# Kernel tuning notes

Hardware: AMD Instinct MI355X
Metric: run time of the kernel (lower is better)

Reference implementation:

```python
import jax, jax.numpy as jnp
import numpy as np

B, N, C, CO = 256, 80, 1024, 1024
SLOPE = 0.2
BN_EPS = 1e-5

def leaky(x):
    return jax.nn.leaky_relu(x, SLOPE)

def setup_inputs() -> dict:
    key = jax.random.key(0)
    ks = jax.random.split(key, 8)
    stdv = 1.0 / np.sqrt(C)
    return {
        "x": jax.random.normal(ks[0], (B, N, C), jnp.float32),
        "out1": jax.random.normal(ks[1], (B, N), jnp.float32),
        "A": jax.random.uniform(ks[2], (N, N), jnp.float32, 0.05, 1.0),
        "static_weight": jax.random.uniform(ks[3], (C, C), jnp.float32, -stdv, stdv),
        "conv_g_w": jax.random.normal(ks[4], (C, C), jnp.float32) * 0.02,
        "conv_g_b": jnp.zeros((C,), jnp.float32),
        "bn_gamma": jnp.ones((C,), jnp.float32),
        "bn_beta": jnp.zeros((C,), jnp.float32),
        "conv_co_w": jax.random.normal(ks[5], (N, 2 * C), jnp.float32) * 0.02,
        "conv_co_b": jnp.zeros((N,), jnp.float32),
        "dynamic_weight": jax.random.uniform(ks[6], (C, CO), jnp.float32, -stdv, stdv),
    }

def _gen_adj(A):
    # D = diag(rowsum(A)^-0.5); adj = (A @ D).T @ D = D A^T D
    d = jnp.power(A.sum(1), -0.5)
    return d[:, None] * A.T * d[None, :]

def _gen_adjs(A):
    # batched version of _gen_adj; A: [B,N,N]
    d = jnp.power(A.sum(2), -0.5)  # [B,N]
    return d[:, :, None] * jnp.swapaxes(A, 1, 2) * d[:, None, :]

def reference(x, out1, A, static_weight, conv_g_w, conv_g_b, bn_gamma, bn_beta, conv_co_w, conv_co_b, dynamic_weight):
    n = x.shape[1]
    # static GCN + residual
    adj_s = _gen_adj(A)
    h = leaky(jnp.einsum('ij,bjc->bic', adj_s, x))
    x = x + h @ static_weight
    # construct dynamic graph
    xt = jnp.swapaxes(x, 1, 2)                      # [B,C,N]
    glb = xt.mean(2)                                # adaptive avg pool -> [B,C]
    glb = glb @ conv_g_w.T + conv_g_b               # 1x1 conv
    mu = glb.mean(0)
    var = glb.var(0)                                # biased, training-mode BN
    glb = (glb - mu) * jax.lax.rsqrt(var + BN_EPS) * bn_gamma + bn_beta
    glb = leaky(glb)
    cat = jnp.concatenate([jnp.broadcast_to(glb[:, :, None], xt.shape), xt], axis=1)  # [B,2C,N]
    dyn = jax.nn.sigmoid(jnp.einsum('nk,bkm->bnm', conv_co_w, cat) + conv_co_b[None, :, None])  # [B,N,N]
    # adjacency consistency loss
    out1s = jax.nn.sigmoid(out1)
    t = jnp.einsum('bn,bnm->bm', out1s, dyn) / n
    loss = jnp.sum(jnp.linalg.norm(out1s - t, axis=1))
    # dynamic GCN
    adjs = _gen_adjs(dyn)
    h = leaky(jnp.einsum('bnm,bmc->bnc', adjs, x))
    out = leaky(h @ dynamic_weight)
    return out, loss
```

## Files before the change

### kernel.cpp

```cpp
#include <hip/hip_runtime.h>
#include <hip/hip_bf16.h>
#include <math.h>

#define B_  256
#define N_  80
#define C_  1024
#define CO_ 1024

typedef __hip_bfloat16 bf16;
using bf16x8 = __attribute__((ext_vector_type(8))) short;
using f32x4  = __attribute__((ext_vector_type(4))) float;

__device__ __forceinline__ float leaky(float v){ return v >= 0.f ? v : 0.2f * v; }
__device__ __forceinline__ float sigmoidf_(float v){ return 1.f / (1.f + __expf(-v)); }

__device__ __forceinline__ void gll16(const void* g, void* l){
    __builtin_amdgcn_global_load_lds(
        (const __attribute__((address_space(1))) void*)g,
        (__attribute__((address_space(3))) void*)l, 16, 0, 0);
}

__global__ __launch_bounds__(256) void k_convT2(const float* __restrict__ W0, const float* __restrict__ W1,
                                                bf16* __restrict__ T0, bf16* __restrict__ T1){
    __shared__ float t[32][33];
    const float* W = blockIdx.z ? W1 : W0;
    bf16* WT = blockIdx.z ? T1 : T0;
    int k0 = blockIdx.y * 32, n0 = blockIdx.x * 32;
    int tx = threadIdx.x & 31, ty = threadIdx.x >> 5;
    for (int i = ty; i < 32; i += 8) t[i][tx] = W[(size_t)(k0 + i) * 1024 + n0 + tx];
    __syncthreads();
    for (int i = ty; i < 32; i += 8)
        WT[(size_t)(n0 + i) * 1024 + k0 + tx] = __float2bfloat16(t[tx][i]);
}

__global__ void k_cvt_ccw(const float* __restrict__ ccw, bf16* __restrict__ ccwb){
    int i = blockIdx.x * 256 + threadIdx.x;
    ccwb[i] = __float2bfloat16(ccw[i]);
}
__global__ void k_cvt4(const float* __restrict__ src, bf16* __restrict__ dst){
    int i = (blockIdx.x * 256 + threadIdx.x) * 4;
    float4 v = *(const float4*)(src + i);
    dst[i + 0] = __float2bfloat16(v.x);
    dst[i + 1] = __float2bfloat16(v.y);
    dst[i + 2] = __float2bfloat16(v.z);
    dst[i + 3] = __float2bfloat16(v.w);
}

__global__ void k_adj(const float* __restrict__ A, bf16* __restrict__ adjb){
    __shared__ float d[N_];
    int t = threadIdx.x;
    if (t < N_){
        float s = 0.f;
        for (int j = 0; j < N_; j++) s += A[t * N_ + j];
        d[t] = rsqrtf(s);
    }
    __syncthreads();
    for (int idx = t; idx < N_ * N_; idx += 256){
        int i = idx / N_, j = idx - i * N_;
        adjb[i * 88 + j] = __float2bfloat16(d[i] * A[j * N_ + i] * d[j]);
    }
}

template<int MODE>
__global__ __launch_bounds__(128) void k_prop_mfma(const void* __restrict__ srcv,
                                                   const bf16* __restrict__ Ag_,
                                                   bf16* __restrict__ H){
    __shared__ bf16 Btl[128 * 88];
    __shared__ bf16 Al [80 * 88];
    int b = blockIdx.x, c0 = blockIdx.y * 128, tid = threadIdx.x;
    int wave = tid >> 6, lane = tid & 63;
    int l15 = lane & 15, hi = lane >> 4;

    const bf16* Ag = Ag_ + (MODE ? (size_t)b * 80 * 88 : 0);
    #pragma unroll
    for (int k = 0; k < 7; k++){
        int cb = k * 128 + wave * 64;
        if (cb + lane < 880)
            gll16(Ag + (size_t)(cb + lane) * 8, Al + (size_t)cb * 8);
    }
    {
        size_t rowbase = (size_t)b * 81920 + c0 + tid;
        #pragma unroll 8
        for (int m = 0; m < 80; m++){
            bf16 h;
            if (MODE == 0) h = __float2bfloat16(((const float*)srcv)[rowbase + (size_t)m * 1024]);
            else           h = ((const bf16*)srcv)[rowbase + (size_t)m * 1024];
            Btl[tid * 88 + m] = h;
        }
    }
    __syncthreads();

    f32x4 acc[5][4];
    #pragma unroll
    for (int i = 0; i < 5; i++)
        #pragma unroll
        for (int j = 0; j < 4; j++) acc[i][j] = (f32x4){0.f, 0.f, 0.f, 0.f};

    #pragma unroll
    for (int ks = 0; ks < 3; ks++){
        bf16x8 a[5], bv[4];
        if (ks < 2){
            int k0 = ks * 32;
            #pragma unroll
            for (int i = 0; i < 5; i++)
                a[i] = *(const bf16x8*)(Al + (i * 16 + l15) * 88 + k0 + hi * 8);
            #pragma unroll
            for (int j = 0; j < 4; j++)
                bv[j] = *(const bf16x8*)(Btl + (wave * 64 + j * 16 + l15) * 88 + k0 + hi * 8);
        } else {
            int koff = (hi < 2) ? 64 + hi * 8 : 0;
            #pragma unroll
            for (int i = 0; i < 5; i++){
                bf16x8 v = *(const bf16x8*)(Al + (i * 16 + l15) * 88 + koff);
                if (hi >= 2) v = 0;
                a[i] = v;
            }
            #pragma unroll
            for (int j = 0; j < 4; j++){
                bf16x8 v = *(const bf16x8*)(Btl + (wave * 64 + j * 16 + l15) * 88 + koff);
                if (hi >= 2) v = 0;
                bv[j] = v;
            }
        }
        #pragma unroll
        for (int i = 0; i < 5; i++)
            #pragma unroll
            for (int j = 0; j < 4; j++)
                acc[i][j] = __builtin_amdgcn_mfma_f32_16x16x32_bf16(a[i], bv[j], acc[i][j], 0, 0, 0);
    }

    #pragma unroll
    for (int i = 0; i < 5; i++){
        #pragma unroll
        for (int r = 0; r < 4; r++){
            int orow = i * 16 + hi * 4 + r;
            #pragma unroll
            for (int j = 0; j < 4; j++){
                int ocol = c0 + wave * 64 + j * 16 + l15;
                H[(size_t)b * 81920 + (size_t)orow * 1024 + ocol] =
                    __float2bfloat16(leaky(acc[i][j][r]));
            }
        }
    }
}

template<int EPI>
__global__ __launch_bounds__(256, 4) void k_gemm_mfma(const bf16* __restrict__ Abf,
                                                      const bf16* __restrict__ WT,
                                                      const float* __restrict__ Res,
                                                      void* __restrict__ Outv){
    __shared__ alignas(16) bf16 As[3][128 * 32];
    __shared__ alignas(16) bf16 Bs[2][128 * 32];
    const int K = 1024;
    const int NT = 32;
    int tid = threadIdx.x;
    int wave = tid >> 6, lane = tid & 63;
    int l15 = lane & 15, hi = lane >> 4;

    int bid = blockIdx.x;
    int xcd = bid & 7, idx = bid >> 3;
    int row0 = (xcd * 20 + (idx >> 3)) * 128;
    int col0 = (idx & 7) * 128;

    int sr = tid >> 2;
    int sq = (tid & 3) ^ ((tid >> 3) & 3);
    const bf16* gA = Abf + (size_t)(row0 + sr) * K + sq * 8;
    const bf16* gB = WT  + (size_t)(col0 + sr) * K + sq * 8;

    int wr = (wave >> 1) * 64, wc = (wave & 1) * 64;
    int soff = (hi ^ ((l15 >> 1) & 3)) * 8;

    f32x4 acc[4][4];
    #pragma unroll
    for (int i = 0; i < 4; i++)
        #pragma unroll
        for (int j = 0; j < 4; j++) acc[i][j] = (f32x4){0.f, 0.f, 0.f, 0.f};

    auto STAGE_A = [&](int t){
        bf16* da = &As[t % 3][wave * 512];
        gll16(gA + t * 32, da);
        gll16(gA + (size_t)64 * K + t * 32, da + 2048);
    };
    auto STAGE_B = [&](int t){
        bf16* db = &Bs[t & 1][wave * 512];
        gll16(gB + t * 32, db);
        gll16(gB + (size_t)64 * K + t * 32, db + 2048);
    };

    STAGE_A(0); STAGE_B(0); STAGE_A(1);
    for (int t = 0; t < NT; ++t){
        if (t < NT - 1) asm volatile("s_waitcnt vmcnt(2)" ::: "memory");
        else            asm volatile("s_waitcnt vmcnt(0)" ::: "memory");
        __builtin_amdgcn_s_barrier();
        if (t + 1 < NT) STAGE_B(t + 1);
        if (t + 2 < NT) STAGE_A(t + 2);
        const bf16* pa = &As[t % 3][0] + (wr + l15) * 32 + soff;
        const bf16* pb = &Bs[t & 1][0] + (wc + l15) * 32 + soff;
        bf16x8 a[4], b[4];
        #pragma unroll
        for (int i = 0; i < 4; i++) a[i] = *(const bf16x8*)(pa + i * 512);
        #pragma unroll
        for (int j = 0; j < 4; j++) b[j] = *(const bf16x8*)(pb + j * 512);
        __builtin_amdgcn_s_setprio(1);
        #pragma unroll
        for (int i = 0; i < 4; i++)
            #pragma unroll
            for (int j = 0; j < 4; j++)
                acc[i][j] = __builtin_amdgcn_mfma_f32_16x16x32_bf16(a[i], b[j], acc[i][j], 0, 0, 0);
        __builtin_amdgcn_s_setprio(0);
    }

    int orow = row0 + wr + hi * 4;
    int ocol = col0 + wc + l15;
    #pragma unroll
    for (int i = 0; i < 4; i++){
        #pragma unroll
        for (int r = 0; r < 4; r++){
            int rr = orow + i * 16 + r;
            #pragma unroll
            for (int j = 0; j < 4; j++){
                size_t o = (size_t)rr * 1024 + ocol + j * 16;
                float v = acc[i][j][r];
                if (EPI == 0) ((bf16*)Outv)[o] = __float2bfloat16(v + Res[o]);
                else          ((float*)Outv)[o] = leaky(v);
            }
        }
    }
}

__global__ __launch_bounds__(256) void k_gemm_glb(const bf16* __restrict__ Abf,
                                                  const bf16* __restrict__ Bw,
                                                  const float* __restrict__ bias,
                                                  float* __restrict__ Out){
    __shared__ alignas(16) bf16 As[3][128 * 32];
    __shared__ alignas(16) bf16 Bs[3][128 * 32];
    const int K = 1024;
    const int NT = 32;
    int tid = threadIdx.x;
    int wave = tid >> 6, lane = tid & 63;
    int l15 = lane & 15, hi = lane >> 4;

    int row0 = (blockIdx.x >> 3) * 128;
    int col0 = (blockIdx.x & 7) * 128;

    int sr = tid >> 2;
    int sq = (tid & 3) ^ ((tid >> 3) & 3);
    const bf16* gA = Abf + (size_t)(row0 + sr) * K + sq * 8;
    const bf16* gB = Bw  + (size_t)(col0 + sr) * K + sq * 8;

    int wr = (wave >> 1) * 64, wc = (wave & 1) * 64;
    int soff = (hi ^ ((l15 >> 1) & 3)) * 8;

    f32x4 acc[4][4];
    #pragma unroll
    for (int i = 0; i < 4; i++)
        #pragma unroll
        for (int j = 0; j < 4; j++) acc[i][j] = (f32x4){0.f, 0.f, 0.f, 0.f};

    auto STAGE = [&](int t){
        int buf = t % 3;
        int k0 = t * 32;
        bf16* da = &As[buf][wave * 512];
        bf16* db = &Bs[buf][wave * 512];
        gll16(gA + k0, da);
        gll16(gA + (size_t)64 * K + k0, da + 2048);
        gll16(gB + k0, db);
        gll16(gB + (size_t)64 * K + k0, db + 2048);
    };

    STAGE(0);
    STAGE(1);
    for (int t = 0; t < NT; ++t){
        if (t == NT - 1) asm volatile("s_waitcnt vmcnt(0)" ::: "memory");
        else             asm volatile("s_waitcnt vmcnt(4)" ::: "memory");
        __builtin_amdgcn_s_barrier();
        if (t + 2 < NT) STAGE(t + 2);
        int buf = t % 3;
        const bf16* pa = &As[buf][0] + (wr + l15) * 32 + soff;
        const bf16* pb = &Bs[buf][0] + (wc + l15) * 32 + soff;
        bf16x8 a[4], b[4];
        #pragma unroll
        for (int i = 0; i < 4; i++) a[i] = *(const bf16x8*)(pa + i * 512);
        #pragma unroll
        for (int j = 0; j < 4; j++) b[j] = *(const bf16x8*)(pb + j * 512);
        #pragma unroll
        for (int i = 0; i < 4; i++)
            #pragma unroll
            for (int j = 0; j < 4; j++)
                acc[i][j] = __builtin_amdgcn_mfma_f32_16x16x32_bf16(a[i], b[j], acc[i][j], 0, 0, 0);
    }

    int orow = row0 + wr + hi * 4;
    int ocol = col0 + wc + l15;
    #pragma unroll
    for (int i = 0; i < 4; i++){
        #pragma unroll
        for (int r = 0; r < 4; r++){
            int rr = orow + i * 16 + r;
            #pragma unroll
            for (int j = 0; j < 4; j++){
                int cl = ocol + j * 16;
                Out[(size_t)rr * 1024 + cl] = acc[i][j][r] + bias[cl];
            }
        }
    }
}

__global__ __launch_bounds__(128) void k_pool(const bf16* __restrict__ X2b, bf16* __restrict__ glb0b){
    int b = blockIdx.x, c8 = threadIdx.x * 8;
    const bf16* p = X2b + (size_t)b * 81920 + c8;
    float s[8] = {0.f,0.f,0.f,0.f,0.f,0.f,0.f,0.f};
    for (int nn = 0; nn < N_; nn++){
        union { bf16x8 v; bf16 e[8]; } u;
        u.v = *(const bf16x8*)(p + (size_t)nn * 1024);
        #pragma unroll
        for (int k = 0; k < 8; k++) s[k] += __bfloat162float(u.e[k]);
    }
    #pragma unroll
    for (int k = 0; k < 8; k++)
        glb0b[b * C_ + c8 + k] = __float2bfloat16(s[k] * (1.f / N_));
}

__global__ __launch_bounds__(256) void k_bnstat(const float* __restrict__ g, float* __restrict__ mu,
                                                float* __restrict__ rstd){
    __shared__ float rs[8][32], rs2[8][32];
    int tid = threadIdx.x;
    int c = blockIdx.x * 32 + (tid & 31);
    int grp = tid >> 5;
    float s = 0.f, s2 = 0.f;
    for (int bb = 0; bb < 32; bb++){
        float v = g[(size_t)(grp * 32 + bb) * 1024 + c];
        s += v; s2 += v * v;
    }
    rs[grp][tid & 31] = s;
    rs2[grp][tid & 31] = s2;
    __syncthreads();
    if (tid < 32){
        float S = 0.f, S2 = 0.f;
        #pragma unroll
        for (int q = 0; q < 8; q++){ S += rs[q][tid]; S2 += rs2[q][tid]; }
        float m = S * (1.f / B_);
        float var = S2 * (1.f / B_) - m * m;
        int cc = blockIdx.x * 32 + tid;
        mu[cc] = m;
        rstd[cc] = rsqrtf(var + 1e-5f);
    }
}

__global__ void k_bnapply(const float* __restrict__ g, const float* __restrict__ mu,
                          const float* __restrict__ rstd, const float* __restrict__ gamma,
                          const float* __restrict__ beta, bf16* __restrict__ o){
    int i = blockIdx.x * 256 + threadIdx.x;
    int c = i & (C_ - 1);
    float v = (g[i] - mu[c]) * rstd[c] * gamma[c] + beta[c];
    o[i] = __float2bfloat16(leaky(v));
}

__global__ __launch_bounds__(320) void k_dyn_fused(const bf16* __restrict__ X2b,
                                                   const bf16* __restrict__ ccwb,
                                                   const bf16* __restrict__ glb2b,
                                                   const float* __restrict__ ccb,
                                                   const float* __restrict__ out1,
                                                   bf16* __restrict__ ADJD,
                                                   float* __restrict__ lossp){
    __shared__ float S[80][81];
    __shared__ float di_s[80], o1s[80], dd[80];
    int b = blockIdx.x, tid = threadIdx.x;
    int wave = tid >> 6, lane = tid & 63;
    int l15 = lane & 15, hi = lane >> 4;

    const bf16* arow = ccwb + (size_t)(wave * 16 + l15) * 2048 + hi * 8;
    const bf16* gG = glb2b + (size_t)b * 1024 + hi * 8;
    const bf16* gX = X2b + (size_t)b * 81920 + hi * 8;

    f32x4 acc[5];
    #pragma unroll
    for (int j = 0; j < 5; j++) acc[j] = (f32x4){0.f, 0.f, 0.f, 0.f};

    #pragma unroll 8
    for (int k0 = 0; k0 < 1024; k0 += 32){
        bf16x8 a = *(const bf16x8*)(arow + k0);
        bf16x8 g = *(const bf16x8*)(gG + k0);
        #pragma unroll
        for (int j = 0; j < 5; j++)
            acc[j] = __builtin_amdgcn_mfma_f32_16x16x32_bf16(a, g, acc[j], 0, 0, 0);
    }
    #pragma unroll 4
    for (int k0 = 0; k0 < 1024; k0 += 32){
        bf16x8 a = *(const bf16x8*)(arow + 1024 + k0);
        #pragma unroll
        for (int j = 0; j < 5; j++){
            bf16x8 bv = *(const bf16x8*)(gX + (size_t)(j * 16 + l15) * 1024 + k0);
            acc[j] = __builtin_amdgcn_mfma_f32_16x16x32_bf16(a, bv, acc[j], 0, 0, 0);
        }
    }

    #pragma unroll
    for (int r = 0; r < 4; r++){
        int n = wave * 16 + hi * 4 + r;
        float cb = ccb[n];
        #pragma unroll
        for (int j = 0; j < 5; j++)
            S[n][j * 16 + l15] = sigmoidf_(acc[j][r] + cb);
    }
    __syncthreads();
    if (tid < 80){
        float rsum = 0.f;
        for (int m = 0; m < 80; m++) rsum += S[tid][m];
        di_s[tid] = rsqrtf(rsum);
        o1s[tid] = sigmoidf_(out1[b * 80 + tid]);
    }
    __syncthreads();
    if (tid < 80){
        float cs = 0.f;
        for (int n = 0; n < 80; n++) cs += o1s[n] * S[n][tid];
        float diff = o1s[tid] - cs * (1.f / 80.f);
        dd[tid] = diff * diff;
    }
    __syncthreads();
    if (tid == 0){
        float s = 0.f;
        for (int m = 0; m < 80; m++) s += dd[m];
        lossp[b] = sqrtf(s);
    }
    bf16* ab = ADJD + (size_t)b * 80 * 88;
    for (int idx = tid; idx < 6400; idx += 320){
        int n = idx / 80, m = idx - n * 80;
        ab[n * 88 + m] = __float2bfloat16(di_s[n] * S[m][n] * di_s[m]);
    }
}

__global__ void k_lsum(const float* __restrict__ lossp, float* __restrict__ out_loss){
    float v = lossp[threadIdx.x];
    for (int off = 32; off; off >>= 1) v += __shfl_down(v, off);
    __shared__ float wsum[4];
    int lane = threadIdx.x & 63, w = threadIdx.x >> 6;
    if (lane == 0) wsum[w] = v;
    __syncthreads();
    if (threadIdx.x == 0) out_loss[0] = wsum[0] + wsum[1] + wsum[2] + wsum[3];
}

extern "C" void kernel_launch(void* const* d_in, const int* in_sizes, int n_in,
                              void* d_out, int out_size, void* d_ws, size_t ws_size,
                              hipStream_t stream) {
    const float* x     = (const float*)d_in[0];
    const float* out1  = (const float*)d_in[1];
    const float* A     = (const float*)d_in[2];
    const float* sw    = (const float*)d_in[3];
    const float* cgw   = (const float*)d_in[4];
    const float* cgb   = (const float*)d_in[5];
    const float* gamma = (const float*)d_in[6];
    const float* beta  = (const float*)d_in[7];
    const float* ccw   = (const float*)d_in[8];
    const float* ccb   = (const float*)d_in[9];
    const float* dw    = (const float*)d_in[10];
    float* out = (float*)d_out;

    const size_t XN = (size_t)B_ * N_ * C_;
    char* p = (char*)d_ws;
    bf16*  Hbf  = (bf16*)p;   p += XN * 2;
    bf16*  X2b  = (bf16*)p;   p += XN * 2;
    bf16*  SWT  = (bf16*)p;   p += (size_t)C_ * C_ * 2;
    bf16*  DWT  = (bf16*)p;   p += (size_t)C_ * CO_ * 2;
    bf16*  CCWB = (bf16*)p;   p += (size_t)N_ * 2048 * 2;
    bf16*  CGWB = (bf16*)p;   p += (size_t)C_ * C_ * 2;
    bf16*  ADJS = (bf16*)p;   p += (size_t)80 * 88 * 2;
    bf16*  ADJD = (bf16*)p;   p += (size_t)B_ * 80 * 88 * 2;
    bf16*  GLB0 = (bf16*)p;   p += (size_t)B_ * C_ * 2;
    float* GLB1 = (float*)p;  p += (size_t)B_ * C_ * 4;
    bf16*  GLB2 = (bf16*)p;   p += (size_t)B_ * C_ * 2;
    float* MU   = (float*)p;  p += C_ * 4;
    float* RSTD = (float*)p;  p += C_ * 4;
    float* LOSSP= (float*)p;  p += B_ * 4;

    k_convT2<<<dim3(32, 32, 2), 256, 0, stream>>>(sw, dw, SWT, DWT);
    k_cvt_ccw<<<(N_ * 2048) / 256, 256, 0, stream>>>(ccw, CCWB);
    k_cvt4<<<(C_ * C_) / 1024, 256, 0, stream>>>(cgw, CGWB);
    k_adj<<<1, 256, 0, stream>>>(A, ADJS);
    k_prop_mfma<0><<<dim3(B_, 8), 128, 0, stream>>>(x, ADJS, Hbf);
    k_gemm_mfma<0><<<1280, 256, 0, stream>>>(Hbf, SWT, x, X2b);
    k_pool<<<B_, 128, 0, stream>>>(X2b, GLB0);
    k_gemm_glb<<<16, 256, 0, stream>>>(GLB0, CGWB, cgb, GLB1);
    k_bnstat<<<32, 256, 0, stream>>>(GLB1, MU, RSTD);
    k_bnapply<<<(B_ * C_) / 256, 256, 0, stream>>>(GLB1, MU, RSTD, gamma, beta, GLB2);
    k_dyn_fused<<<B_, 320, 0, stream>>>(X2b, CCWB, GLB2, ccb, out1, ADJD, LOSSP);
    k_lsum<<<1, 256, 0, stream>>>(LOSSP, out + (size_t)B_ * N_ * CO_);
    k_prop_mfma<1><<<dim3(B_, 8), 128, 0, stream>>>(X2b, ADJD, Hbf);
    k_gemm_mfma<1><<<1280, 256, 0, stream>>>(Hbf, DWT, nullptr, out);
}
```

Before: 273.1 us.

## Fuse dynamic adjacency construction with dynamic graph propagation in one kernel

Merges the dynamic adjacency kernel and the second propagation kernel: each batch block builds the normalized adjacency in LDS and then loops over all 1024 channels in 128-wide chunks to compute leaky(adj @ x) directly into H. This removes the ADJD global round-trip and one launch. The cost is only 256 blocks of 512 threads, each serially walking 8 channel chunks, so parallelism drops from 2048 blocks and three waves sit idle during the adjacency GEMM. It also adds an unroll pragma to the pooling loop.

```diff
diff --git a/kernel.cpp b/kernel.cpp
--- a/kernel.cpp
+++ b/kernel.cpp
@@ -61,17 +61,15 @@
     }
 }
 
-template<int MODE>
-__global__ __launch_bounds__(128) void k_prop_mfma(const void* __restrict__ srcv,
-                                                   const bf16* __restrict__ Ag_,
-                                                   bf16* __restrict__ H){
+__global__ __launch_bounds__(128) void k_prop_static(const float* __restrict__ xsrc,
+                                                     const bf16* __restrict__ Ag,
+                                                     bf16* __restrict__ H){
     __shared__ bf16 Btl[128 * 88];
     __shared__ bf16 Al [80 * 88];
     int b = blockIdx.x, c0 = blockIdx.y * 128, tid = threadIdx.x;
     int wave = tid >> 6, lane = tid & 63;
     int l15 = lane & 15, hi = lane >> 4;
 
-    const bf16* Ag = Ag_ + (MODE ? (size_t)b * 80 * 88 : 0);
     #pragma unroll
     for (int k = 0; k < 7; k++){
         int cb = k * 128 + wave * 64;
@@ -81,12 +79,8 @@
     {
         size_t rowbase = (size_t)b * 81920 + c0 + tid;
         #pragma unroll 8
-        for (int m = 0; m < 80; m++){
-            bf16 h;
-            if (MODE == 0) h = __float2bfloat16(((const float*)srcv)[rowbase + (size_t)m * 1024]);
-            else           h = ((const bf16*)srcv)[rowbase + (size_t)m * 1024];
-            Btl[tid * 88 + m] = h;
-        }
+        for (int m = 0; m < 80; m++)
+            Btl[tid * 88 + m] = __float2bfloat16(xsrc[rowbase + (size_t)m * 1024]);
     }
     __syncthreads();
 
@@ -310,6 +304,7 @@
     int b = blockIdx.x, c8 = threadIdx.x * 8;
     const bf16* p = X2b + (size_t)b * 81920 + c8;
     float s[8] = {0.f,0.f,0.f,0.f,0.f,0.f,0.f,0.f};
+    #pragma unroll 8
     for (int nn = 0; nn < N_; nn++){
         union { bf16x8 v; bf16 e[8]; } u;
         u.v = *(const bf16x8*)(p + (size_t)nn * 1024);
@@ -356,77 +351,117 @@
     o[i] = __float2bfloat16(leaky(v));
 }
 
-__global__ __launch_bounds__(320) void k_dyn_fused(const bf16* __restrict__ X2b,
-                                                   const bf16* __restrict__ ccwb,
-                                                   const bf16* __restrict__ glb2b,
-                                                   const float* __restrict__ ccb,
-                                                   const float* __restrict__ out1,
-                                                   bf16* __restrict__ ADJD,
-                                                   float* __restrict__ lossp){
-    __shared__ float S[80][81];
+__global__ __launch_bounds__(512) void k_dyn_prop(const bf16* __restrict__ X2b,
+                                                  const bf16* __restrict__ ccwb,
+                                                  const bf16* __restrict__ glb2b,
+                                                  const float* __restrict__ ccb,
+                                                  const float* __restrict__ out1,
+                                                  bf16* __restrict__ H,
+                                                  float* __restrict__ lossp){
+    __shared__ char uSb[80 * 81 * 4];
+    __shared__ bf16 ADJ[80 * 90];
     __shared__ float di_s[80], o1s[80], dd[80];
+    float* S = (float*)uSb;
+    bf16* Btl = (bf16*)uSb;
     int b = blockIdx.x, tid = threadIdx.x;
     int wave = tid >> 6, lane = tid & 63;
     int l15 = lane & 15, hi = lane >> 4;
 
-    const bf16* arow = ccwb + (size_t)(wave * 16 + l15) * 2048 + hi * 8;
-    const bf16* gG = glb2b + (size_t)b * 1024 + hi * 8;
-    const bf16* gX = X2b + (size_t)b * 81920 + hi * 8;
-
-    f32x4 acc[5];
-    #pragma unroll
-    for (int j = 0; j < 5; j++) acc[j] = (f32x4){0.f, 0.f, 0.f, 0.f};
-
-    #pragma unroll 8
-    for (int k0 = 0; k0 < 1024; k0 += 32){
-        bf16x8 a = *(const bf16x8*)(arow + k0);
-        bf16x8 g = *(const bf16x8*)(gG + k0);
-        #pragma unroll
-        for (int j = 0; j < 5; j++)
-            acc[j] = __builtin_amdgcn_mfma_f32_16x16x32_bf16(a, g, acc[j], 0, 0, 0);
-    }
-    #pragma unroll 4
-    for (int k0 = 0; k0 < 1024; k0 += 32){
-        bf16x8 a = *(const bf16x8*)(arow + 1024 + k0);
-        #pragma unroll
-        for (int j = 0; j < 5; j++){
-            bf16x8 bv = *(const bf16x8*)(gX + (size_t)(j * 16 + l15) * 1024 + k0);
-            acc[j] = __builtin_amdgcn_mfma_f32_16x16x32_bf16(a, bv, acc[j], 0, 0, 0);
-        }
-    }
-
-    #pragma unroll
-    for (int r = 0; r < 4; r++){
-        int n = wave * 16 + hi * 4 + r;
-        float cb = ccb[n];
-        #pragma unroll
-        for (int j = 0; j < 5; j++)
-            S[n][j * 16 + l15] = sigmoidf_(acc[j][r] + cb);
+    if (wave < 5){
+        const bf16* arow = ccwb + (size_t)(wave * 16 + l15) * 2048 + hi * 8;
+        const bf16* gG = glb2b + (size_t)b * 1024 + hi * 8;
+        const bf16* gX = X2b + (size_t)b * 81920 + hi * 8;
+        f32x4 acc[5];
+        #pragma unroll
+        for (int j = 0; j < 5; j++) acc[j] = (f32x4){0.f, 0.f, 0.f, 0.f};
+        #pragma unroll 8
+        for (int k0 = 0; k0 < 1024; k0 += 32){
+            bf16x8 a = *(const bf16x8*)(arow + k0);
+            bf16x8 g = *(const bf16x8*)(gG + k0);
+            #pragma unroll
+            for (int j = 0; j < 5; j++)
+                acc[j] = __builtin_amdgcn_mfma_f32_16x16x32_bf16(a, g, acc[j], 0, 0, 0);
+        }
+        #pragma unroll 4
+        for (int k0 = 0; k0 < 1024; k0 += 32){
+            bf16x8 a = *(const bf16x8*)(arow + 1024 + k0);
+            #pragma unroll
+            for (int j = 0; j < 5; j++){
+                bf16x8 bv = *(const bf16x8*)(gX + (size_t)(j * 16 + l15) * 1024 + k0);
+                acc[j] = __builtin_amdgcn_mfma_f32_16x16x32_bf16(a, bv, acc[j], 0, 0, 0);
+            }
+        }
+        #pragma unroll
+        for (int r = 0; r < 4; r++){
+            int n = wave * 16 + hi * 4 + r;
+            float cb = ccb[n];
+            #pragma unroll
+            for (int j = 0; j < 5; j++)
+                S[n * 81 + j * 16 + l15] = sigmoidf_(acc[j][r] + cb);
+        }
     }
     __syncthreads();
     if (tid < 80){
         float rsum = 0.f;
-        for (int m = 0; m < 80; m++) rsum += S[tid][m];
+        #pragma unroll 8
+        for (int m = 0; m < 80; m++) rsum += S[tid * 81 + m];
         di_s[tid] = rsqrtf(rsum);
         o1s[tid] = sigmoidf_(out1[b * 80 + tid]);
     }
     __syncthreads();
     if (tid < 80){
         float cs = 0.f;
-        for (int n = 0; n < 80; n++) cs += o1s[n] * S[n][tid];
+        #pragma unroll 8
+        for (int n = 0; n < 80; n++) cs += o1s[n] * S[n * 81 + tid];
         float diff = o1s[tid] - cs * (1.f / 80.f);
         dd[tid] = diff * diff;
     }
     __syncthreads();
+    for (int idx = tid; idx < 6400; idx += 512){
+        int n = idx / 80, m = idx - n * 80;
+        ADJ[n * 90 + m] = __float2bfloat16(di_s[n] * S[m * 81 + n] * di_s[m]);
+    }
     if (tid == 0){
         float s = 0.f;
         for (int m = 0; m < 80; m++) s += dd[m];
         lossp[b] = sqrtf(s);
     }
-    bf16* ab = ADJD + (size_t)b * 80 * 88;
-    for (int idx = tid; idx < 6400; idx += 320){
-        int n = idx / 80, m = idx - n * 80;
-        ab[n * 88 + m] = __float2bfloat16(di_s[n] * S[m][n] * di_s[m]);
+    for (int c0 = 0; c0 < 1024; c0 += 128){
+        __syncthreads();
+        {
+            int cc = tid & 127, g = tid >> 7;
+            const bf16* src = X2b + (size_t)b * 81920 + c0 + cc;
+            #pragma unroll 5
+            for (int m = g * 20; m < g * 20 + 20; m++)
+                Btl[cc * 90 + m] = src[(size_t)m * 1024];
+        }
+        __syncthreads();
+        f32x4 pacc[5];
+        #pragma unroll
+        for (int i = 0; i < 5; i++) pacc[i] = (f32x4){0.f, 0.f, 0.f, 0.f};
+        #pragma unroll
+        for (int ks = 0; ks < 3; ks++){
+            int koff = (ks < 2) ? ks * 32 + hi * 8 : ((hi < 2) ? 64 + hi * 8 : 0);
+            bool dead = (ks == 2) && (hi >= 2);
+            bf16x8 bv = *(const bf16x8*)(Btl + (wave * 16 + l15) * 90 + koff);
+            if (dead) bv = 0;
+            #pragma unroll
+            for (int i = 0; i < 5; i++){
+                bf16x8 a = *(const bf16x8*)(ADJ + (i * 16 + l15) * 90 + koff);
+                if (dead) a = 0;
+                pacc[i] = __builtin_amdgcn_mfma_f32_16x16x32_bf16(a, bv, pacc[i], 0, 0, 0);
+            }
+        }
+        #pragma unroll
+        for (int i = 0; i < 5; i++){
+            #pragma unroll
+            for (int r = 0; r < 4; r++){
+                int n = i * 16 + hi * 4 + r;
+                int col = c0 + wave * 16 + l15;
+                H[(size_t)b * 81920 + (size_t)n * 1024 + col] =
+                    __float2bfloat16(leaky(pacc[i][r]));
+            }
+        }
     }
 }
 
@@ -465,7 +500,6 @@
     bf16*  CCWB = (bf16*)p;   p += (size_t)N_ * 2048 * 2;
     bf16*  CGWB = (bf16*)p;   p += (size_t)C_ * C_ * 2;
     bf16*  ADJS = (bf16*)p;   p += (size_t)80 * 88 * 2;
-    bf16*  ADJD = (bf16*)p;   p += (size_t)B_ * 80 * 88 * 2;
     bf16*  GLB0 = (bf16*)p;   p += (size_t)B_ * C_ * 2;
     float* GLB1 = (float*)p;  p += (size_t)B_ * C_ * 4;
     bf16*  GLB2 = (bf16*)p;   p += (size_t)B_ * C_ * 2;
@@ -477,14 +511,13 @@
     k_cvt_ccw<<<(N_ * 2048) / 256, 256, 0, stream>>>(ccw, CCWB);
     k_cvt4<<<(C_ * C_) / 1024, 256, 0, stream>>>(cgw, CGWB);
     k_adj<<<1, 256, 0, stream>>>(A, ADJS);
-    k_prop_mfma<0><<<dim3(B_, 8), 128, 0, stream>>>(x, ADJS, Hbf);
+    k_prop_static<<<dim3(B_, 8), 128, 0, stream>>>(x, ADJS, Hbf);
     k_gemm_mfma<0><<<1280, 256, 0, stream>>>(Hbf, SWT, x, X2b);
     k_pool<<<B_, 128, 0, stream>>>(X2b, GLB0);
     k_gemm_glb<<<16, 256, 0, stream>>>(GLB0, CGWB, cgb, GLB1);
     k_bnstat<<<32, 256, 0, stream>>>(GLB1, MU, RSTD);
     k_bnapply<<<(B_ * C_) / 256, 256, 0, stream>>>(GLB1, MU, RSTD, gamma, beta, GLB2);
-    k_dyn_fused<<<B_, 320, 0, stream>>>(X2b, CCWB, GLB2, ccb, out1, ADJD, LOSSP);
+    k_dyn_prop<<<B_, 512, 0, stream>>>(X2b, CCWB, GLB2, ccb, out1, Hbf, LOSSP);
     k_lsum<<<1, 256, 0, stream>>>(LOSSP, out + (size_t)B_ * N_ * CO_);
-    k_prop_mfma<1><<<dim3(B_, 8), 128, 0, stream>>>(X2b, ADJD, Hbf);
     k_gemm_mfma<1><<<1280, 256, 0, stream>>>(Hbf, DWT, nullptr, out);
 }
```

After: 271.9 us. Within noise of the previous version (-0.4%).
